# Performance work log

Hardware: AMD Instinct MI355X
Metric: run time of the kernel (lower is better)

Reference implementation:

```python
import jax, jax.numpy as jnp
import numpy as np

SCALE = 8.0  # (dim // n_heads) ** 0.5 = (1024 // 16) ** 0.5


def setup_inputs() -> dict:
    key = jax.random.key(0)
    kq, kk, kv = jax.random.split(key, 3)
    shape = (2, 16, 2048, 64)  # [B, H, N, Dh]
    q = jax.random.normal(kq, shape, dtype=jnp.float32)
    k = jax.random.normal(kk, shape, dtype=jnp.float32)
    v = jax.random.normal(kv, shape, dtype=jnp.float32)
    return {"q": q, "k": k, "v": v}


def reference(q, k, v):
    # scores[b,h,n,m] = sum_d q[b,h,n,d] * k[b,h,m,d], then MULTIPLIED by scale
    # (the original multiplies by sqrt(head_dim), it does not divide).
    scores = jnp.einsum('bhnd,bhmd->bhnm', q, k) * SCALE
    scores = jax.nn.softmax(scores, axis=-1)
    # Faithful to the original quirky einsum: sums over n (query axis), keeps m.
    # out[b,h,m,d] = (sum_n scores[b,h,n,m]) * v[b,h,m,d]
    out = jnp.einsum('bhnm,bhmd->bhmd', scores, v)
    return out
```

## Files before the change

kernel.cpp:

```cpp
#include <hip/hip_runtime.h>
#include <math.h>

#define BH 32
#define NN 2048
#define DD 64
#define BHNN (BH * NN)
#define QK ((size_t)BH * NN * DD)

#define QSCALE 11.5415603f

typedef __attribute__((ext_vector_type(8)))  _Float16 halfx8;
typedef __attribute__((ext_vector_type(4)))  _Float16 halfx4;
typedef __attribute__((ext_vector_type(16))) float    floatx16;

__device__ inline float fexp2(float x) { return __builtin_amdgcn_exp2f(x); }
__device__ inline float flog2(float x) { return __builtin_amdgcn_logf(x); }

__device__ inline int rowmap(int r, int half) {
    return (r & 3) + 8 * (r >> 2) + 4 * half;
}

__global__ __launch_bounds__(256) void convert_kernel(const float4* __restrict__ q,
                                                      const float4* __restrict__ k,
                                                      _Float16* __restrict__ qhi,
                                                      _Float16* __restrict__ khi) {
    size_t gid = (size_t)blockIdx.x * 256 + threadIdx.x;
    float4 qa = q[gid];
    float4 ka = k[gid];
    float qf[4] = {qa.x, qa.y, qa.z, qa.w};
    float kf[4] = {ka.x, ka.y, ka.z, ka.w};
    halfx4 h, kh;
#pragma unroll
    for (int i = 0; i < 4; ++i) {
        h[i]  = (_Float16)(qf[i] * QSCALE);
        kh[i] = (_Float16)kf[i];
    }
    *(halfx4*)&qhi[gid * 4] = h;
    size_t rowbase = (gid * 4) & ~(size_t)63;
    int j = (int)((gid >> 1) & 7) ^ (int)((gid >> 4) & 7);
    *(halfx4*)&khi[rowbase + (size_t)(j << 3) + ((gid & 1) << 2)] = kh;
}

__device__ inline void stage_tile_async(const _Float16* __restrict__ gtile,
                                        _Float16* lds, int wave, int lane) {
#pragma unroll
    for (int i = 0; i < 4; ++i) {
        const char* gp = (const char*)gtile + wave * 4096 + i * 1024 + lane * 16;
        char* lp = (char*)lds + wave * 4096 + i * 1024;
        __builtin_amdgcn_global_load_lds(
            (const __attribute__((address_space(1))) unsigned int*)gp,
            (__attribute__((address_space(3))) unsigned int*)lp, 16, 0, 0);
    }
}

__device__ inline void load_a(const _Float16* __restrict__ qhi_row,
                              int half, halfx8 ah[4]) {
#pragma unroll
    for (int ks = 0; ks < 4; ++ks)
        ah[ks] = *(const halfx8*)&qhi_row[ks * 16 + half * 8];
}

__global__ __launch_bounds__(256, 4) void stats_kernel(const _Float16* __restrict__ qhi,
                                                       const _Float16* __restrict__ khi,
                                                       float* __restrict__ smax_p,
                                                       float* __restrict__ sden_p) {
    __shared__ _Float16 K2[2 * 128 * 64];
    const int g    = blockIdx.x & 63;
    const int bh   = g & 31;
    const int ms   = g >> 5;
    const int n0   = (blockIdx.x >> 6) * 128;
    const int tid  = threadIdx.x;
    const int wave = tid >> 6, lane = tid & 63;
    const int half = lane >> 5, l31 = lane & 31;
    const int xr   = l31 & 7;
    const size_t base = (size_t)bh * NN * DD;

    const _Float16* khi_b = khi + base;
    stage_tile_async(khi_b + (size_t)(ms * 8) * 8192, K2, wave, lane);

    halfx8 ah[4];
    {
        size_t ro = base + (size_t)(n0 + wave * 32 + l31) * DD;
        load_a(qhi + ro, half, ah);
    }

    float m_run[16], d_run[16];
#pragma unroll
    for (int r = 0; r < 16; ++r) { m_run[r] = -INFINITY; d_run[r] = 0.f; }

    __syncthreads();

#pragma unroll 1
    for (int mti = 0; mti < 8; ++mti) {
        const _Float16* Kc = K2 + (mti & 1) * 8192;
        if (mti < 7)
            stage_tile_async(khi_b + (size_t)(ms * 8 + mti + 1) * 8192,
                             K2 + ((mti + 1) & 1) * 8192, wave, lane);

#pragma unroll 1
        for (int p = 0; p < 2; ++p) {
            floatx16 acc[2];
#pragma unroll
            for (int t = 0; t < 2; ++t)
#pragma unroll
                for (int e = 0; e < 16; ++e) acc[t][e] = 0.f;

#pragma unroll
            for (int tt = 0; tt < 2; ++tt) {
                const int mr = (p * 2 + tt) * 32 + l31;
                const _Float16* rowp = Kc + (size_t)mr * 64;
#pragma unroll
                for (int ks = 0; ks < 4; ++ks) {
                    const int j = (ks * 2 + half) ^ xr;
                    halfx8 bhf = *(const halfx8*)&rowp[j << 3];
                    acc[tt] = __builtin_amdgcn_mfma_f32_32x32x16_f16(ah[ks], bhf, acc[tt], 0, 0, 0);
                }
            }

#pragma unroll
            for (int r = 0; r < 16; ++r) {
                float tmax = fmaxf(acc[0][r], acc[1][r]);
                float m_new = fmaxf(m_run[r], tmax);
                float s = fexp2(acc[0][r] - m_new) + fexp2(acc[1][r] - m_new);
                d_run[r] = d_run[r] * fexp2(m_run[r] - m_new) + s;
                m_run[r] = m_new;
            }
        }

        if (mti < 7) __syncthreads();
    }

    float* smp = smax_p + ((size_t)ms * BH + bh) * NN;
    float* sdp = sden_p + ((size_t)ms * BH + bh) * NN;
#pragma unroll
    for (int r = 0; r < 16; ++r) {
        float M = m_run[r];
#pragma unroll
        for (int off = 1; off < 32; off <<= 1)
            M = fmaxf(M, __shfl_xor(M, off));
        float dd = d_run[r] * fexp2(m_run[r] - M);
#pragma unroll
        for (int off = 1; off < 32; off <<= 1)
            dd += __shfl_xor(dd, off);
        if (l31 == 0) {
            int row = n0 + wave * 32 + rowmap(r, half);
            smp[row] = M;
            sdp[row] = dd;
        }
    }
}

__global__ __launch_bounds__(256, 4) void wsum_kernel(const _Float16* __restrict__ qhi,
                                                      const _Float16* __restrict__ khi,
                                                      const float* __restrict__ smax_p,
                                                      const float* __restrict__ sden_p,
                                                      float* __restrict__ wpart) {
    __shared__ _Float16 Khi[128 * 64];
    __shared__ float wred[4 * 128];
    __shared__ float Ms[1024];
    const int g    = blockIdx.x & 63;
    const int bh   = g & 31;
    const int nz   = g >> 5;
    const int m0   = (blockIdx.x >> 6) * 128;
    const int tid  = threadIdx.x;
    const int wave = tid >> 6, lane = tid & 63;
    const int half = lane >> 5, l31 = lane & 31;
    const int xr   = l31 & 7;
    const size_t base = (size_t)bh * NN * DD;

    stage_tile_async(khi + base + (size_t)m0 * 64, Khi, wave, lane);

    {
        size_t roff = (size_t)bh * NN + nz * 1024 + tid * 4;
        float4 m0v = *(const float4*)&smax_p[roff];
        float4 m1v = *(const float4*)&smax_p[(size_t)BHNN + roff];
        float4 d0v = *(const float4*)&sden_p[roff];
        float4 d1v = *(const float4*)&sden_p[(size_t)BHNN + roff];
        float mm0[4] = {m0v.x, m0v.y, m0v.z, m0v.w};
        float mm1[4] = {m1v.x, m1v.y, m1v.z, m1v.w};
        float dd0[4] = {d0v.x, d0v.y, d0v.z, d0v.w};
        float dd1[4] = {d1v.x, d1v.y, d1v.z, d1v.w};
#pragma unroll
        for (int j = 0; j < 4; ++j) {
            float M = fmaxf(mm0[j], mm1[j]);
            float den = dd0[j] * fexp2(mm0[j] - M) + dd1[j] * fexp2(mm1[j] - M);
            Ms[tid * 4 + j] = M + flog2(den);
        }
    }
    __syncthreads();

    float wacc0 = 0.f, wacc1 = 0.f, wacc2 = 0.f, wacc3 = 0.f;

#pragma unroll 1
    for (int it = 0; it < 8; ++it) {
        const int ls = wave + it * 4;
        halfx8 ah[4];
        {
            size_t ro = base + (size_t)((nz * 32 + ls) * 32 + l31) * DD;
            load_a(qhi + ro, half, ah);
        }

#pragma unroll 1
        for (int p = 0; p < 2; ++p) {
            floatx16 acc[2];
#pragma unroll
            for (int t = 0; t < 2; ++t)
#pragma unroll
                for (int e = 0; e < 16; ++e) acc[t][e] = 0.f;

#pragma unroll
            for (int tt = 0; tt < 2; ++tt) {
                const int mr = (p * 2 + tt) * 32 + l31;
                const _Float16* rowp = Khi + (size_t)mr * 64;
#pragma unroll
                for (int ks = 0; ks < 4; ++ks) {
                    const int j = (ks * 2 + half) ^ xr;
                    halfx8 bhf = *(const halfx8*)&rowp[j << 3];
                    acc[tt] = __builtin_amdgcn_mfma_f32_32x32x16_f16(ah[ks], bhf, acc[tt], 0, 0, 0);
                }
            }

            float w0 = 0.f, w1 = 0.f;
#pragma unroll
            for (int r = 0; r < 16; ++r) {
                const int lrow = ls * 32 + rowmap(r, half);
                float Madj = Ms[lrow];
                w0 += fexp2(acc[0][r] - Madj);
                w1 += fexp2(acc[1][r] - Madj);
            }
            if (p == 0) { wacc0 += w0; wacc1 += w1; }
            else        { wacc2 += w0; wacc3 += w1; }
        }
    }

    float wacc[4] = {wacc0, wacc1, wacc2, wacc3};
#pragma unroll
    for (int t = 0; t < 4; ++t) wacc[t] += __shfl_xor(wacc[t], 32);
    if (half == 0) {
#pragma unroll
        for (int t = 0; t < 4; ++t) wred[wave * 128 + t * 32 + l31] = wacc[t];
    }
    __syncthreads();
    if (tid < 128) {
        float s = wred[tid] + wred[128 + tid] + wred[256 + tid] + wred[384 + tid];
        wpart[((size_t)nz * BH + bh) * NN + m0 + tid] = s;
    }
}

__global__ __launch_bounds__(256) void out_kernel(const float* __restrict__ v,
                                                  const float* __restrict__ w0,
                                                  const float* __restrict__ w1,
                                                  float* __restrict__ out) {
    size_t gid = (size_t)blockIdx.x * 256 + threadIdx.x;
    const float4* v4 = (const float4*)v;
    float4* o4 = (float4*)out;
    float4 vv = v4[gid];
    float ww = w0[gid >> 4] + w1[gid >> 4];
    o4[gid] = make_float4(vv.x * ww, vv.y * ww, vv.z * ww, vv.w * ww);
}

extern "C" void kernel_launch(void* const* d_in, const int* in_sizes, int n_in,
                              void* d_out, int out_size, void* d_ws, size_t ws_size,
                              hipStream_t stream) {
    const float* q = (const float*)d_in[0];
    const float* k = (const float*)d_in[1];
    const float* v = (const float*)d_in[2];
    float* out = (float*)d_out;

    _Float16* qhi = (_Float16*)d_ws;
    _Float16* khi = qhi + QK;
    float* smax_p = (float*)(khi + QK);
    float* sden_p = smax_p + 2 * BHNN;
    float* wpart  = sden_p + 2 * BHNN;

    convert_kernel<<<QK / 4 / 256, 256, 0, stream>>>((const float4*)q, (const float4*)k,
                                                     qhi, khi);
    stats_kernel<<<1024, 256, 0, stream>>>(qhi, khi, smax_p, sden_p);
    wsum_kernel<<<1024, 256, 0, stream>>>(qhi, khi, smax_p, sden_p, wpart);
    out_kernel<<<(BH * NN * DD / 4) / 256, 256, 0, stream>>>(v, wpart, wpart + BHNN, out);
}
```

Before: 160.7 us.

## Fuse output scaling into wsum kernel with 512-thread blocks covering full query range

The wsum kernel now uses 512-thread blocks (8 waves) that each cover all 2048 query rows for a 128-key tile, instead of splitting queries across two blocks. This removes the partial-sum buffer and lets the block multiply v by the final column weight and write the output directly, eliminating the separate out_kernel launch and the wpart round trip. In exchange, the grid halves to 512 blocks, and launch_bounds(512,4) may constrain registers and occupancy more tightly.

```diff
diff --git a/kernel.cpp b/kernel.cpp
--- a/kernel.cpp
+++ b/kernel.cpp
@@ -41,12 +41,23 @@
     *(halfx4*)&khi[rowbase + (size_t)(j << 3) + ((gid & 1) << 2)] = kh;
 }
 
-__device__ inline void stage_tile_async(const _Float16* __restrict__ gtile,
-                                        _Float16* lds, int wave, int lane) {
+__device__ inline void stage_tile_async4(const _Float16* __restrict__ gtile,
+                                         _Float16* lds, int wave, int lane) {
 #pragma unroll
     for (int i = 0; i < 4; ++i) {
         const char* gp = (const char*)gtile + wave * 4096 + i * 1024 + lane * 16;
         char* lp = (char*)lds + wave * 4096 + i * 1024;
+        __builtin_amdgcn_global_load_lds(
+            (const __attribute__((address_space(1))) unsigned int*)gp,
+            (__attribute__((address_space(3))) unsigned int*)lp, 16, 0, 0);
+    }
+}
+__device__ inline void stage_tile_async8(const _Float16* __restrict__ gtile,
+                                         _Float16* lds, int wave, int lane) {
+#pragma unroll
+    for (int i = 0; i < 2; ++i) {
+        const char* gp = (const char*)gtile + wave * 2048 + i * 1024 + lane * 16;
+        char* lp = (char*)lds + wave * 2048 + i * 1024;
         __builtin_amdgcn_global_load_lds(
             (const __attribute__((address_space(1))) unsigned int*)gp,
             (__attribute__((address_space(3))) unsigned int*)lp, 16, 0, 0);
@@ -76,7 +87,7 @@
     const size_t base = (size_t)bh * NN * DD;
 
     const _Float16* khi_b = khi + base;
-    stage_tile_async(khi_b + (size_t)(ms * 8) * 8192, K2, wave, lane);
+    stage_tile_async4(khi_b + (size_t)(ms * 8) * 8192, K2, wave, lane);
 
     halfx8 ah[4];
     {
@@ -94,8 +105,8 @@
     for (int mti = 0; mti < 8; ++mti) {
         const _Float16* Kc = K2 + (mti & 1) * 8192;
         if (mti < 7)
-            stage_tile_async(khi_b + (size_t)(ms * 8 + mti + 1) * 8192,
-                             K2 + ((mti + 1) & 1) * 8192, wave, lane);
+            stage_tile_async4(khi_b + (size_t)(ms * 8 + mti + 1) * 8192,
+                              K2 + ((mti + 1) & 1) * 8192, wave, lane);
 
 #pragma unroll 1
         for (int p = 0; p < 2; ++p) {
@@ -150,28 +161,29 @@
     }
 }
 
-__global__ __launch_bounds__(256, 4) void wsum_kernel(const _Float16* __restrict__ qhi,
+__global__ __launch_bounds__(512, 4) void wsum_kernel(const _Float16* __restrict__ qhi,
                                                       const _Float16* __restrict__ khi,
                                                       const float* __restrict__ smax_p,
                                                       const float* __restrict__ sden_p,
-                                                      float* __restrict__ wpart) {
+                                                      const float* __restrict__ v,
+                                                      float* __restrict__ out) {
     __shared__ _Float16 Khi[128 * 64];
-    __shared__ float wred[4 * 128];
-    __shared__ float Ms[1024];
-    const int g    = blockIdx.x & 63;
-    const int bh   = g & 31;
-    const int nz   = g >> 5;
-    const int m0   = (blockIdx.x >> 6) * 128;
+    __shared__ float Ms[2048];
+    __shared__ float wred[8 * 128];
+    __shared__ float wfin[128];
+    const int b    = blockIdx.x;
+    const int bh   = b & 31;
+    const int m0   = (b >> 5) * 128;
     const int tid  = threadIdx.x;
     const int wave = tid >> 6, lane = tid & 63;
     const int half = lane >> 5, l31 = lane & 31;
     const int xr   = l31 & 7;
     const size_t base = (size_t)bh * NN * DD;
 
-    stage_tile_async(khi + base + (size_t)m0 * 64, Khi, wave, lane);
+    stage_tile_async8(khi + base + (size_t)m0 * 64, Khi, wave, lane);
 
     {
-        size_t roff = (size_t)bh * NN + nz * 1024 + tid * 4;
+        size_t roff = (size_t)bh * NN + tid * 4;
         float4 m0v = *(const float4*)&smax_p[roff];
         float4 m1v = *(const float4*)&smax_p[(size_t)BHNN + roff];
         float4 d0v = *(const float4*)&sden_p[roff];
@@ -193,10 +205,10 @@
 
 #pragma unroll 1
     for (int it = 0; it < 8; ++it) {
-        const int ls = wave + it * 4;
+        const int ls = wave + it * 8;
         halfx8 ah[4];
         {
-            size_t ro = base + (size_t)((nz * 32 + ls) * 32 + l31) * DD;
+            size_t ro = base + (size_t)(ls * 32 + l31) * DD;
             load_a(qhi + ro, half, ah);
         }
 
@@ -242,21 +254,22 @@
     }
     __syncthreads();
     if (tid < 128) {
-        float s = wred[tid] + wred[128 + tid] + wred[256 + tid] + wred[384 + tid];
-        wpart[((size_t)nz * BH + bh) * NN + m0 + tid] = s;
-    }
-}
-
-__global__ __launch_bounds__(256) void out_kernel(const float* __restrict__ v,
-                                                  const float* __restrict__ w0,
-                                                  const float* __restrict__ w1,
-                                                  float* __restrict__ out) {
-    size_t gid = (size_t)blockIdx.x * 256 + threadIdx.x;
-    const float4* v4 = (const float4*)v;
-    float4* o4 = (float4*)out;
-    float4 vv = v4[gid];
-    float ww = w0[gid >> 4] + w1[gid >> 4];
-    o4[gid] = make_float4(vv.x * ww, vv.y * ww, vv.z * ww, vv.w * ww);
+        float s = 0.f;
+#pragma unroll
+        for (int w = 0; w < 8; ++w) s += wred[w * 128 + tid];
+        wfin[tid] = s;
+    }
+    __syncthreads();
+
+    const float4* v4 = (const float4*)(v + base + (size_t)m0 * DD);
+    float4* o4 = (float4*)(out + base + (size_t)m0 * DD);
+#pragma unroll
+    for (int i = 0; i < 4; ++i) {
+        int idx = tid + 512 * i;
+        float ww = wfin[idx >> 4];
+        float4 vv = v4[idx];
+        o4[idx] = make_float4(vv.x * ww, vv.y * ww, vv.z * ww, vv.w * ww);
+    }
 }
 
 extern "C" void kernel_launch(void* const* d_in, const int* in_sizes, int n_in,
@@ -271,11 +284,9 @@
     _Float16* khi = qhi + QK;
     float* smax_p = (float*)(khi + QK);
     float* sden_p = smax_p + 2 * BHNN;
-    float* wpart  = sden_p + 2 * BHNN;
 
     convert_kernel<<<QK / 4 / 256, 256, 0, stream>>>((const float4*)q, (const float4*)k,
                                                      qhi, khi);
     stats_kernel<<<1024, 256, 0, stream>>>(qhi, khi, smax_p, sden_p);
-    wsum_kernel<<<1024, 256, 0, stream>>>(qhi, khi, smax_p, sden_p, wpart);
-    out_kernel<<<(BH * NN * DD / 4) / 256, 256, 0, stream>>>(v, wpart, wpart + BHNN, out);
-}
+    wsum_kernel<<<512, 512, 0, stream>>>(qhi, khi, smax_p, sden_p, v, out);
+}
```

Result: no change. 159.5 us (-0.7%).
